# Kernel optimization log

Hardware: AMD Instinct MI355X
Metric: run time of the kernel (lower is better)

The kernel has to match this reference:

```python
import jax, jax.numpy as jnp
import numpy as np
from math import sqrt

B, L, D_MODEL = 4, 128, 256
V, D_WORD = 50257, 768
H = 8  # n_heads; d_keys = D_MODEL // H = 32


def setup_inputs() -> dict:
    key = jax.random.key(0)
    ks = jax.random.split(key, 10)
    s = lambda k, shape, fan: jax.random.normal(k, shape, dtype=jnp.float32) / np.sqrt(fan)
    return {
        "time_series_embedding": jax.random.normal(ks[0], (B, L, D_MODEL), dtype=jnp.float32),
        "word_embedding": jax.random.normal(ks[1], (V, D_WORD), dtype=jnp.float32) * 0.02,
        "Wq": s(ks[2], (D_MODEL, D_MODEL), D_MODEL),
        "bq": jnp.zeros((D_MODEL,), jnp.float32),
        "Wk": s(ks[3], (D_WORD, D_MODEL), D_WORD),
        "bk": jnp.zeros((D_MODEL,), jnp.float32),
        "Wv": s(ks[4], (D_WORD, D_MODEL), D_WORD),
        "bv": jnp.zeros((D_MODEL,), jnp.float32),
        "Wo": s(ks[5], (D_MODEL, D_MODEL), D_MODEL),
        "bo": jnp.zeros((D_MODEL,), jnp.float32),
    }


def reference(time_series_embedding, word_embedding, Wq, bq, Wk, bk, Wv, bv, Wo, bo):
    b, l, _ = time_series_embedding.shape
    v, _ = word_embedding.shape
    h = H
    e = D_MODEL // h
    # projections
    query = (time_series_embedding @ Wq + bq).reshape(b, l, h, e)   # [B,L,H,E]
    key = (word_embedding @ Wk + bk).reshape(v, h, e)               # [V,H,E]
    value = (word_embedding @ Wv + bv).reshape(v, h, e)             # [V,H,E]
    scale = 1.0 / sqrt(e)
    # scores over full vocab: [B,H,V,L]
    scores = jnp.einsum('blhe,vhe->bhvl', query, key)
    # NOTE: faithful to source -- softmax over the LAST axis (l, the query dim)
    attn = jax.nn.softmax(scale * scores, axis=-1)
    # dropout is identity in eval mode
    reprog = jnp.einsum('bhvl,vhe->blhe', attn, value).reshape(b, l, h * e)
    return reprog @ Wo + bo  # [B,L,d_model]
```

## Files before the change

kernel.cpp:

```cpp
#include <hip/hip_runtime.h>
#include <hip/hip_bf16.h>
#include <string.h>

#define BB 4
#define LL 128
#define DM 256
#define VV 50257
#define VPAD 50304
#define DW 768
#define HH 8
#define EE 32

typedef __attribute__((ext_vector_type(8))) short sh8;
typedef __attribute__((ext_vector_type(4))) short sh4;
typedef __attribute__((ext_vector_type(4))) float f32x4;

static __device__ inline unsigned short bfbits(float x) {
  __hip_bfloat16 h = __float2bfloat16(x);
  unsigned short u;
  __builtin_memcpy(&u, &h, 2);
  return u;
}

#define GLDS16(gsrc, ldst)                                                    \
  __builtin_amdgcn_global_load_lds(                                          \
      (const __attribute__((address_space(1))) void*)(gsrc),                 \
      (__attribute__((address_space(3))) void*)(ldst), 16, 0, 0)

#define WAIT_VM(N)                                                           \
  asm volatile("s_waitcnt vmcnt(" #N ")" ::: "memory");                      \
  __builtin_amdgcn_sched_barrier(0)
#define WAIT_LGKM0                                                           \
  asm volatile("s_waitcnt lgkmcnt(0)" ::: "memory");                         \
  __builtin_amdgcn_sched_barrier(0)

__global__ __launch_bounds__(256) void prep_kernel(
    const float* __restrict__ Wk, const float* __restrict__ Wv,
    unsigned short* __restrict__ Wkt, unsigned short* __restrict__ Wvt,
    const float* __restrict__ tse, const float* __restrict__ Wq,
    const float* __restrict__ bq, unsigned short* __restrict__ Qb) {
  __shared__ float tileS[64][65];
  int bid = blockIdx.x;
  int t = threadIdx.x;
  if (bid < 96) {
    int z = bid / 48, rem = bid - z * 48;
    int x = rem % 12, y = rem / 12;
    const float* src = z ? Wv : Wk;
    unsigned short* dst = z ? Wvt : Wkt;
    int k0 = x * 64, n0 = y * 64;
    int c = t & 63, rb = t >> 6;
#pragma unroll
    for (int j = 0; j < 16; ++j) {
      int r = j * 4 + rb;
      tileS[r][c] = src[(size_t)(k0 + r) * DM + n0 + c];
    }
    __syncthreads();
#pragma unroll
    for (int j = 0; j < 16; ++j) {
      int r = j * 4 + rb;
      dst[(size_t)(n0 + r) * DW + k0 + c] = bfbits(tileS[c][r]);
    }
  } else {
    int r = bid - 96;
    int n = t;
    float* row = &tileS[0][0];
    row[n] = tse[r * DM + n];
    __syncthreads();
    float acc = bq[n];
#pragma unroll 8
    for (int k = 0; k < DM; ++k)
      acc = fmaf(row[k], Wq[k * DM + n], acc);
    const float scale = 0.17677669529663687f * 1.4426950408889634f;
    Qb[r * DM + n] = bfbits(acc * scale);
  }
}

__global__ __launch_bounds__(256, 2) void kvproj_kernel(
    const float* __restrict__ WE, const unsigned short* __restrict__ Wkt,
    const unsigned short* __restrict__ Wvt, const float* __restrict__ bk,
    const float* __restrict__ bv, unsigned short* __restrict__ Kb,
    unsigned short* __restrict__ Vb) {
  __shared__ float WEf[2][128 * 32];
  __shared__ short Kbuf[2][128 * 32];
  __shared__ short Vbuf[2][128 * 32];

  int bx = blockIdx.x;
  int v0 = (bx >> 1) * 128;
  int colbase = (bx & 1) * 128;
  int t = threadIdx.x;
  int w = t >> 6, lane = t & 63, a = lane & 15, quad = lane >> 4;
  int wm = w >> 1, wn = w & 1;

  auto stage = [&](int kt, int p) {
#pragma unroll
    for (int i = 0; i < 4; ++i) {
      int s = w * 256 + i * 64 + lane;
      int row = s >> 3;
      int cc = (s & 7) ^ (row & 7);
      int grow = v0 + row;
      if (grow > VV - 1) grow = VV - 1;
      GLDS16(WE + (size_t)grow * DW + kt * 32 + cc * 4,
             &WEf[p][(w * 256 + i * 64) * 4]);
    }
#pragma unroll
    for (int i = 0; i < 2; ++i) {
      int s = w * 128 + i * 64 + lane;
      int row = s >> 2;
      int cc = (s & 3) ^ ((row >> 1) & 3);
      GLDS16(Wkt + (size_t)(colbase + row) * DW + kt * 32 + cc * 8,
             &Kbuf[p][(w * 128 + i * 64) * 8]);
      GLDS16(Wvt + (size_t)(colbase + row) * DW + kt * 32 + cc * 8,
             &Vbuf[p][(w * 128 + i * 64) * 8]);
    }
  };

  f32x4 Ck[4][4], Cv[4][4];
#pragma unroll
  for (int mb = 0; mb < 4; ++mb)
#pragma unroll
    for (int nb = 0; nb < 4; ++nb) {
      Ck[mb][nb] = (f32x4){0.f, 0.f, 0.f, 0.f};
      Cv[mb][nb] = (f32x4){0.f, 0.f, 0.f, 0.f};
    }

  stage(0, 0);
  stage(1, 1);

  for (int kt = 0; kt < 24; ++kt) {
    int p = kt & 1;
    if (kt < 23) {
      WAIT_VM(8);
    } else {
      WAIT_VM(0);
    }
    __builtin_amdgcn_s_barrier();
    __builtin_amdgcn_sched_barrier(0);

    sh8 A[4], Bk[4], Bv[4];
#pragma unroll
    for (int mb = 0; mb < 4; ++mb) {
      int row = wm * 64 + mb * 16 + a;
      const float* rp = &WEf[p][row * 32];
      f32x4 lo = *(const f32x4*)(rp + ((2 * quad) ^ (a & 7)) * 4);
      f32x4 hi = *(const f32x4*)(rp + ((2 * quad + 1) ^ (a & 7)) * 4);
      sh4 l4 = {(short)bfbits(lo[0]), (short)bfbits(lo[1]),
                (short)bfbits(lo[2]), (short)bfbits(lo[3])};
      sh4 h4 = {(short)bfbits(hi[0]), (short)bfbits(hi[1]),
                (short)bfbits(hi[2]), (short)bfbits(hi[3])};
      A[mb] = __builtin_shufflevector(l4, h4, 0, 1, 2, 3, 4, 5, 6, 7);
    }
#pragma unroll
    for (int nb = 0; nb < 4; ++nb) {
      int krow = (wn * 4 + nb) * 16 + a;
      int cp = (quad ^ ((krow >> 1) & 3)) * 8;
      Bk[nb] = *(const sh8*)&Kbuf[p][krow * 32 + cp];
      Bv[nb] = *(const sh8*)&Vbuf[p][krow * 32 + cp];
    }
#pragma unroll
    for (int mb = 0; mb < 4; ++mb)
#pragma unroll
      for (int nb = 0; nb < 4; ++nb) {
        Ck[mb][nb] = __builtin_amdgcn_mfma_f32_16x16x32_bf16(
            A[mb], Bk[nb], Ck[mb][nb], 0, 0, 0);
        Cv[mb][nb] = __builtin_amdgcn_mfma_f32_16x16x32_bf16(
            A[mb], Bv[nb], Cv[mb][nb], 0, 0, 0);
      }

    WAIT_LGKM0;
    __builtin_amdgcn_s_barrier();
    __builtin_amdgcn_sched_barrier(0);
    if (kt < 22) stage(kt + 2, p);
  }

  float bkv[4], bvv[4];
#pragma unroll
  for (int nb = 0; nb < 4; ++nb) {
    int n = colbase + (wn * 4 + nb) * 16 + a;
    bkv[nb] = bk[n];
    bvv[nb] = bv[n];
  }
#pragma unroll
  for (int mb = 0; mb < 4; ++mb)
#pragma unroll
    for (int nb = 0; nb < 4; ++nb)
#pragma unroll
      for (int r = 0; r < 4; ++r) {
        int m = v0 + wm * 64 + mb * 16 + quad * 4 + r;
        int n = colbase + (wn * 4 + nb) * 16 + a;
        bool ok = m < VV;
        Kb[(size_t)m * DM + n] = ok ? bfbits(Ck[mb][nb][r] + bkv[nb]) : 0;
        Vb[(size_t)m * DM + n] = ok ? bfbits(Cv[mb][nb][r] + bvv[nb]) : 0;
      }
}

#define PST 72
__global__ __launch_bounds__(256) void attn_kernel(
    const unsigned short* __restrict__ Qb, const unsigned short* __restrict__ Kb,
    const unsigned short* __restrict__ Vb, float* __restrict__ part, int bpb,
    int nc) {
  __shared__ short Pb[LL * PST];
  __shared__ short Vt[EE * PST];

  int bh = blockIdx.x / bpb;
  int chunk = blockIdx.x - bh * bpb;
  int b = bh >> 3, h = bh & 7;
  int t = threadIdx.x;
  int w = t >> 6;
  int lane = t & 63;
  int a = lane & 15;
  int quad = lane >> 4;
  int vr = t >> 2, e0 = (t & 3) * 8;

  sh8 qf[8];
  const unsigned short* qbase = Qb + (size_t)(b * LL) * DM + h * EE;
#pragma unroll
  for (int tau = 0; tau < 8; ++tau)
    qf[tau] = *(const sh8*)(qbase + (size_t)(tau * 16 + a) * DM + quad * 8);

  f32x4 C[2][2];
#pragma unroll
  for (int mb = 0; mb < 2; ++mb)
#pragma unroll
    for (int nb = 0; nb < 2; ++nb)
      C[mb][nb] = (f32x4){0.f, 0.f, 0.f, 0.f};

  const int ntiles = VPAD >> 6;

  sh8 af, vv;
  {
    int v0 = chunk << 6;
    af = *(const sh8*)(Kb + (size_t)(v0 + 16 * w + a) * DM + h * EE + quad * 8);
    vv = *(const sh8*)(Vb + (size_t)(v0 + vr) * DM + h * EE + e0);
  }

  for (int tile = chunk; tile < ntiles; tile += bpb) {
    f32x4 S[8];
#pragma unroll
    for (int tau = 0; tau < 8; ++tau) {
      f32x4 z = {0.f, 0.f, 0.f, 0.f};
      S[tau] = __builtin_amdgcn_mfma_f32_16x16x32_bf16(af, qf[tau], z, 0, 0, 0);
    }

    sh8 af2 = af, vv2 = vv;
    int nt = tile + bpb;
    if (nt < ntiles) {
      int v0n = nt << 6;
      af2 = *(const sh8*)(Kb + (size_t)(v0n + 16 * w + a) * DM + h * EE + quad * 8);
      vv2 = *(const sh8*)(Vb + (size_t)(v0n + vr) * DM + h * EE + e0);
    }

    float sm[4], inv[4];
#pragma unroll
    for (int r = 0; r < 4; ++r) sm[r] = 0.f;
#pragma unroll
    for (int tau = 0; tau < 8; ++tau)
#pragma unroll
      for (int r = 0; r < 4; ++r) {
        float ex = __builtin_amdgcn_exp2f(S[tau][r]);
        S[tau][r] = ex;
        sm[r] += ex;
      }
#pragma unroll
    for (int msk = 1; msk <= 8; msk <<= 1)
#pragma unroll
      for (int r = 0; r < 4; ++r)
        sm[r] += __shfl_xor(sm[r], msk);
#pragma unroll
    for (int r = 0; r < 4; ++r) inv[r] = 1.f / sm[r];

    WAIT_LGKM0;
    __builtin_amdgcn_s_barrier();
    __builtin_amdgcn_sched_barrier(0);

    {
      const short* vs = (const short*)&vv;
#pragma unroll
      for (int j = 0; j < 8; ++j)
        Vt[(e0 + j) * PST + vr] = vs[j];
    }
#pragma unroll
    for (int tau = 0; tau < 8; ++tau) {
      ushort4 pk;
      pk.x = bfbits(S[tau][0] * inv[0]);
      pk.y = bfbits(S[tau][1] * inv[1]);
      pk.z = bfbits(S[tau][2] * inv[2]);
      pk.w = bfbits(S[tau][3] * inv[3]);
      *(ushort4*)&Pb[(tau * 16 + a) * PST + 16 * w + quad * 4] = pk;
    }
    WAIT_LGKM0;
    __builtin_amdgcn_s_barrier();
    __builtin_amdgcn_sched_barrier(0);

    af = af2;
    vv = vv2;

    sh8 Afr[2][2], Bfr[2][2];
#pragma unroll
    for (int mb = 0; mb < 2; ++mb)
#pragma unroll
      for (int kb = 0; kb < 2; ++kb)
        Afr[mb][kb] =
            *(const sh8*)&Pb[(32 * w + mb * 16 + a) * PST + kb * 32 + quad * 8];
#pragma unroll
    for (int kb = 0; kb < 2; ++kb)
#pragma unroll
      for (int nb = 0; nb < 2; ++nb)
        Bfr[kb][nb] = *(const sh8*)&Vt[(nb * 16 + a) * PST + kb * 32 + quad * 8];
#pragma unroll
    for (int kb = 0; kb < 2; ++kb)
#pragma unroll
      for (int mb = 0; mb < 2; ++mb)
#pragma unroll
        for (int nb = 0; nb < 2; ++nb)
          C[mb][nb] = __builtin_amdgcn_mfma_f32_16x16x32_bf16(
              Afr[mb][kb], Bfr[kb][nb], C[mb][nb], 0, 0, 0);
  }

#pragma unroll
  for (int mb = 0; mb < 2; ++mb)
#pragma unroll
    for (int nb = 0; nb < 2; ++nb)
#pragma unroll
      for (int r = 0; r < 4; ++r) {
        int l = 32 * w + mb * 16 + quad * 4 + r;
        int e = nb * 16 + a;
        size_t idx = (size_t)(b * LL + l) * DM + h * EE + e;
        if (nc > 1)
          part[(size_t)chunk * (BB * LL * DM) + idx] = C[mb][nb][r];
        else
          atomicAdd(&part[idx], C[mb][nb][r]);
      }
}

__global__ __launch_bounds__(256) void outproj_kernel(
    const float* __restrict__ part, const float* __restrict__ Wo,
    const float* __restrict__ bo, float* __restrict__ out, int nc) {
  __shared__ float row[DM];
  int r = blockIdx.x, n = threadIdx.x;
  float s = 0.f;
  for (int c = 0; c < nc; ++c)
    s += part[(size_t)c * (BB * LL * DM) + (size_t)r * DM + n];
  row[n] = s;
  __syncthreads();
  float acc = bo[n];
#pragma unroll 8
  for (int k = 0; k < DM; ++k)
    acc = fmaf(row[k], Wo[k * DM + n], acc);
  out[r * DM + n] = acc;
}

extern "C" void kernel_launch(void* const* d_in, const int* in_sizes, int n_in,
                              void* d_out, int out_size, void* d_ws, size_t ws_size,
                              hipStream_t stream) {
  const float* tse = (const float*)d_in[0];
  const float* WE  = (const float*)d_in[1];
  const float* Wq  = (const float*)d_in[2];
  const float* bq  = (const float*)d_in[3];
  const float* Wk  = (const float*)d_in[4];
  const float* bk  = (const float*)d_in[5];
  const float* Wv  = (const float*)d_in[6];
  const float* bv  = (const float*)d_in[7];
  const float* Wo  = (const float*)d_in[8];
  const float* bo  = (const float*)d_in[9];
  float* out = (float*)d_out;

  char* ws = (char*)d_ws;
  const size_t QB_BYTES   = (size_t)BB * LL * DM * 2;
  const size_t KV_BYTES   = (size_t)VPAD * DM * 2;
  const size_t WT_BYTES   = (size_t)DM * DW * 2;
  const size_t PART_BYTES = (size_t)BB * LL * DM * 4;
  unsigned short* Qb  = (unsigned short*)ws;
  unsigned short* Kb  = (unsigned short*)(ws + QB_BYTES);
  unsigned short* Vb  = (unsigned short*)(ws + QB_BYTES + KV_BYTES);
  char* X = ws + QB_BYTES + 2 * KV_BYTES;
  unsigned short* Wkt = (unsigned short*)X;
  unsigned short* Wvt = (unsigned short*)(X + WT_BYTES);
  float* part = (float*)X;

  const int BPB = 32;

  const size_t NEED_PART =
      QB_BYTES + 2 * KV_BYTES + (size_t)BPB * PART_BYTES;
  const int nc = (ws_size >= NEED_PART) ? BPB : 1;

  prep_kernel<<<96 + BB * LL, 256, 0, stream>>>(Wk, Wv, Wkt, Wvt, tse, Wq, bq, Qb);
  kvproj_kernel<<<(VPAD / 128) * 2, 256, 0, stream>>>(WE, Wkt, Wvt, bk, bv, Kb, Vb);
  if (nc == 1)
    (void)hipMemsetAsync(part, 0, PART_BYTES, stream);
  attn_kernel<<<32 * BPB, 256, 0, stream>>>(Qb, Kb, Vb, part, BPB, nc);
  outproj_kernel<<<BB * LL, 256, 0, stream>>>(part, Wo, bo, out, nc);
}
```

Baseline: 401.4 us.

## Restructure K/V projection: direct global A loads, triple-buffered weights, smaller row tiles

The K/V projection kernel no longer stages word-embedding rows through LDS. Each lane loads its fp32 A-fragment straight from global memory and converts it to bf16 in registers. Weight tiles move to a three-slot LDS ring, which removes the second barrier per k-step, and the next stage is issued right after the barrier. The vocab tile drops from 128 to 64 rows, doubling the grid and allowing 3 blocks per CU, at the cost of reloading the weight tiles twice as often and doing uncoalesced-ish direct loads of the embedding.

Result: slower. 461.1 us (+14.9%).

```diff
diff --git a/kernel.cpp b/kernel.cpp
--- a/kernel.cpp
+++ b/kernel.cpp
@@ -28,10 +28,15 @@
       (__attribute__((address_space(3))) void*)(ldst), 16, 0, 0)
 
 #define WAIT_VM(N)                                                           \
+  __builtin_amdgcn_sched_barrier(0);                                         \
   asm volatile("s_waitcnt vmcnt(" #N ")" ::: "memory");                      \
   __builtin_amdgcn_sched_barrier(0)
 #define WAIT_LGKM0                                                           \
   asm volatile("s_waitcnt lgkmcnt(0)" ::: "memory");                         \
+  __builtin_amdgcn_sched_barrier(0)
+#define SBARRIER                                                             \
+  __builtin_amdgcn_sched_barrier(0);                                         \
+  __builtin_amdgcn_s_barrier();                                              \
   __builtin_amdgcn_sched_barrier(0)
 
 __global__ __launch_bounds__(256) void prep_kernel(
@@ -75,33 +80,22 @@
   }
 }
 
-__global__ __launch_bounds__(256, 2) void kvproj_kernel(
+__global__ __launch_bounds__(256, 3) void kvproj_kernel(
     const float* __restrict__ WE, const unsigned short* __restrict__ Wkt,
     const unsigned short* __restrict__ Wvt, const float* __restrict__ bk,
     const float* __restrict__ bv, unsigned short* __restrict__ Kb,
     unsigned short* __restrict__ Vb) {
-  __shared__ float WEf[2][128 * 32];
-  __shared__ short Kbuf[2][128 * 32];
-  __shared__ short Vbuf[2][128 * 32];
+  __shared__ short Kbuf[3][128 * 32];
+  __shared__ short Vbuf[3][128 * 32];
 
   int bx = blockIdx.x;
-  int v0 = (bx >> 1) * 128;
+  int v0 = (bx >> 1) * 64;
   int colbase = (bx & 1) * 128;
   int t = threadIdx.x;
   int w = t >> 6, lane = t & 63, a = lane & 15, quad = lane >> 4;
   int wm = w >> 1, wn = w & 1;
 
-  auto stage = [&](int kt, int p) {
-#pragma unroll
-    for (int i = 0; i < 4; ++i) {
-      int s = w * 256 + i * 64 + lane;
-      int row = s >> 3;
-      int cc = (s & 7) ^ (row & 7);
-      int grow = v0 + row;
-      if (grow > VV - 1) grow = VV - 1;
-      GLDS16(WE + (size_t)grow * DW + kt * 32 + cc * 4,
-             &WEf[p][(w * 256 + i * 64) * 4]);
-    }
+  auto stageKV = [&](int kt, int p) {
 #pragma unroll
     for (int i = 0; i < 2; ++i) {
       int s = w * 128 + i * 64 + lane;
@@ -114,50 +108,71 @@
     }
   };
 
-  f32x4 Ck[4][4], Cv[4][4];
-#pragma unroll
-  for (int mb = 0; mb < 4; ++mb)
+  const float* werow[2];
+#pragma unroll
+  for (int mb = 0; mb < 2; ++mb) {
+    int grow = v0 + wm * 32 + mb * 16 + a;
+    if (grow > VV - 1) grow = VV - 1;
+    werow[mb] = WE + (size_t)grow * DW + quad * 8;
+  }
+
+  f32x4 Ck[2][4], Cv[2][4];
+#pragma unroll
+  for (int mb = 0; mb < 2; ++mb)
 #pragma unroll
     for (int nb = 0; nb < 4; ++nb) {
       Ck[mb][nb] = (f32x4){0.f, 0.f, 0.f, 0.f};
       Cv[mb][nb] = (f32x4){0.f, 0.f, 0.f, 0.f};
     }
 
-  stage(0, 0);
-  stage(1, 1);
-
+  stageKV(0, 0);
+  stageKV(1, 1);
+
+  int p = 0;
   for (int kt = 0; kt < 24; ++kt) {
-    int p = kt & 1;
     if (kt < 23) {
-      WAIT_VM(8);
+      WAIT_VM(4);
     } else {
       WAIT_VM(0);
     }
-    __builtin_amdgcn_s_barrier();
+    SBARRIER;
+
+    f32x4 lo0 = *(const f32x4*)(werow[0] + kt * 32);
+    f32x4 hi0 = *(const f32x4*)(werow[0] + kt * 32 + 4);
+    f32x4 lo1 = *(const f32x4*)(werow[1] + kt * 32);
+    f32x4 hi1 = *(const f32x4*)(werow[1] + kt * 32 + 4);
     __builtin_amdgcn_sched_barrier(0);
 
-    sh8 A[4], Bk[4], Bv[4];
-#pragma unroll
-    for (int mb = 0; mb < 4; ++mb) {
-      int row = wm * 64 + mb * 16 + a;
-      const float* rp = &WEf[p][row * 32];
-      f32x4 lo = *(const f32x4*)(rp + ((2 * quad) ^ (a & 7)) * 4);
-      f32x4 hi = *(const f32x4*)(rp + ((2 * quad + 1) ^ (a & 7)) * 4);
-      sh4 l4 = {(short)bfbits(lo[0]), (short)bfbits(lo[1]),
-                (short)bfbits(lo[2]), (short)bfbits(lo[3])};
-      sh4 h4 = {(short)bfbits(hi[0]), (short)bfbits(hi[1]),
-                (short)bfbits(hi[2]), (short)bfbits(hi[3])};
-      A[mb] = __builtin_shufflevector(l4, h4, 0, 1, 2, 3, 4, 5, 6, 7);
-    }
+    {
+      int q = p - 1;
+      if (q < 0) q = 2;
+      if (kt < 22) stageKV(kt + 2, q);
+    }
+
+    sh8 A[2];
+    {
+      sh4 l4 = {(short)bfbits(lo0[0]), (short)bfbits(lo0[1]),
+                (short)bfbits(lo0[2]), (short)bfbits(lo0[3])};
+      sh4 h4 = {(short)bfbits(hi0[0]), (short)bfbits(hi0[1]),
+                (short)bfbits(hi0[2]), (short)bfbits(hi0[3])};
+      A[0] = __builtin_shufflevector(l4, h4, 0, 1, 2, 3, 4, 5, 6, 7);
+      sh4 l5 = {(short)bfbits(lo1[0]), (short)bfbits(lo1[1]),
+                (short)bfbits(lo1[2]), (short)bfbits(lo1[3])};
+      sh4 h5 = {(short)bfbits(hi1[0]), (short)bfbits(hi1[1]),
+                (short)bfbits(hi1[2]), (short)bfbits(hi1[3])};
+      A[1] = __builtin_shufflevector(l5, h5, 0, 1, 2, 3, 4, 5, 6, 7);
+    }
+
+    sh8 Bk[4], Bv[4];
 #pragma unroll
     for (int nb = 0; nb < 4; ++nb) {
-      int krow = (wn * 4 + nb) * 16 + a;
+      int krow = wn * 64 + nb * 16 + a;
       int cp = (quad ^ ((krow >> 1) & 3)) * 8;
       Bk[nb] = *(const sh8*)&Kbuf[p][krow * 32 + cp];
       Bv[nb] = *(const sh8*)&Vbuf[p][krow * 32 + cp];
     }
 #pragma unroll
-    for (int mb = 0; mb < 4; ++mb)
+    for (int mb = 0; mb < 2; ++mb)
 #pragma unroll
       for (int nb = 0; nb < 4; ++nb) {
         Ck[mb][nb] = __builtin_amdgcn_mfma_f32_16x16x32_bf16(
@@ -166,27 +181,24 @@
             A[mb], Bv[nb], Cv[mb][nb], 0, 0, 0);
       }
 
-    WAIT_LGKM0;
-    __builtin_amdgcn_s_barrier();
-    __builtin_amdgcn_sched_barrier(0);
-    if (kt < 22) stage(kt + 2, p);
+    p = (p == 2) ? 0 : p + 1;
   }
 
   float bkv[4], bvv[4];
 #pragma unroll
   for (int nb = 0; nb < 4; ++nb) {
-    int n = colbase + (wn * 4 + nb) * 16 + a;
+    int n = colbase + wn * 64 + nb * 16 + a;
     bkv[nb] = bk[n];
     bvv[nb] = bv[n];
   }
 #pragma unroll
-  for (int mb = 0; mb < 4; ++mb)
+  for (int mb = 0; mb < 2; ++mb)
 #pragma unroll
     for (int nb = 0; nb < 4; ++nb)
 #pragma unroll
       for (int r = 0; r < 4; ++r) {
-        int m = v0 + wm * 64 + mb * 16 + quad * 4 + r;
-        int n = colbase + (wn * 4 + nb) * 16 + a;
+        int m = v0 + wm * 32 + mb * 16 + quad * 4 + r;
+        int n = colbase + wn * 64 + nb * 16 + a;
         bool ok = m < VV;
         Kb[(size_t)m * DM + n] = ok ? bfbits(Ck[mb][nb][r] + bkv[nb]) : 0;
         Vb[(size_t)m * DM + n] = ok ? bfbits(Cv[mb][nb][r] + bvv[nb]) : 0;
@@ -269,8 +281,7 @@
     for (int r = 0; r < 4; ++r) inv[r] = 1.f / sm[r];
 
     WAIT_LGKM0;
-    __builtin_amdgcn_s_barrier();
-    __builtin_amdgcn_sched_barrier(0);
+    SBARRIER;
 
     {
       const short* vs = (const short*)&vv;
@@ -288,8 +299,7 @@
       *(ushort4*)&Pb[(tau * 16 + a) * PST + 16 * w + quad * 4] = pk;
     }
     WAIT_LGKM0;
-    __builtin_amdgcn_s_barrier();
-    __builtin_amdgcn_sched_barrier(0);
+    SBARRIER;
 
     af = af2;
     vv = vv2;
@@ -384,7 +394,7 @@
   const int nc = (ws_size >= NEED_PART) ? BPB : 1;
 
   prep_kernel<<<96 + BB * LL, 256, 0, stream>>>(Wk, Wv, Wkt, Wvt, tse, Wq, bq, Qb);
-  kvproj_kernel<<<(VPAD / 128) * 2, 256, 0, stream>>>(WE, Wkt, Wvt, bk, bv, Kb, Vb);
+  kvproj_kernel<<<(VPAD / 64) * 2, 256, 0, stream>>>(WE, Wkt, Wvt, bk, bv, Kb, Vb);
   if (nc == 1)
     (void)hipMemsetAsync(part, 0, PART_BYTES, stream);
   attn_kernel<<<32 * BPB, 256, 0, stream>>>(Qb, Kb, Vb, part, BPB, nc);
```

## Store V transposed and keep P in registers for attention PV MFMA

Applied to the files above, without the earlier changes.

The K/V projection kernel now writes V transposed (feature-major over the padded vocab), so the attention kernel can load V fragments straight from global memory. The softmax probabilities stay in registers and feed 16x16x16 bf16 MFMAs directly. This removes the shared-memory staging of P and V and the two block barriers per tile. In exchange, each wave accumulates partial outputs for all 128 queries, which must be reduced across the four waves through shared memory at the end. The kvproj epilogue now does strided 8-byte stores of V^T.

Result: no change. 408.7 us (+1.8%).

```diff
diff --git a/kernel.cpp b/kernel.cpp
--- a/kernel.cpp
+++ b/kernel.cpp
@@ -28,11 +28,29 @@
       (__attribute__((address_space(3))) void*)(ldst), 16, 0, 0)
 
 #define WAIT_VM(N)                                                           \
+  __builtin_amdgcn_sched_barrier(0);                                         \
   asm volatile("s_waitcnt vmcnt(" #N ")" ::: "memory");                      \
   __builtin_amdgcn_sched_barrier(0)
 #define WAIT_LGKM0                                                           \
   asm volatile("s_waitcnt lgkmcnt(0)" ::: "memory");                         \
   __builtin_amdgcn_sched_barrier(0)
+#define SBARRIER                                                             \
+  __builtin_amdgcn_sched_barrier(0);                                         \
+  __builtin_amdgcn_s_barrier();                                              \
+  __builtin_amdgcn_sched_barrier(0)
+
+#if __has_builtin(__builtin_amdgcn_mfma_f32_16x16x16bf16_1k)
+#define MFMA16(A, B, C) __builtin_amdgcn_mfma_f32_16x16x16bf16_1k(A, B, C, 0, 0, 0)
+#elif __has_builtin(__builtin_amdgcn_mfma_f32_16x16x16_bf16)
+#define MFMA16(A, B, C) __builtin_amdgcn_mfma_f32_16x16x16_bf16(A, B, C, 0, 0, 0)
+#else
+static __device__ inline f32x4 mfma16_asm(sh4 a, sh4 b, f32x4 c) {
+  asm volatile("v_mfma_f32_16x16x16_bf16 %0, %1, %2, %0"
+               : "+v"(c) : "v"(a), "v"(b));
+  return c;
+}
+#define MFMA16(A, B, C) mfma16_asm(A, B, C)
+#endif
 
 __global__ __launch_bounds__(256) void prep_kernel(
     const float* __restrict__ Wk, const float* __restrict__ Wv,
@@ -79,7 +97,7 @@
     const float* __restrict__ WE, const unsigned short* __restrict__ Wkt,
     const unsigned short* __restrict__ Wvt, const float* __restrict__ bk,
     const float* __restrict__ bv, unsigned short* __restrict__ Kb,
-    unsigned short* __restrict__ Vb) {
+    unsigned short* __restrict__ Vbt) {
   __shared__ float WEf[2][128 * 32];
   __shared__ short Kbuf[2][128 * 32];
   __shared__ short Vbuf[2][128 * 32];
@@ -133,8 +151,7 @@
     } else {
       WAIT_VM(0);
     }
-    __builtin_amdgcn_s_barrier();
-    __builtin_amdgcn_sched_barrier(0);
+    SBARRIER;
 
     sh8 A[4], Bk[4], Bv[4];
 #pragma unroll
@@ -167,8 +184,7 @@
       }
 
     WAIT_LGKM0;
-    __builtin_amdgcn_s_barrier();
-    __builtin_amdgcn_sched_barrier(0);
+    SBARRIER;
     if (kt < 22) stage(kt + 2, p);
   }
 
@@ -182,24 +198,26 @@
 #pragma unroll
   for (int mb = 0; mb < 4; ++mb)
 #pragma unroll
-    for (int nb = 0; nb < 4; ++nb)
+    for (int nb = 0; nb < 4; ++nb) {
+      int m0 = v0 + wm * 64 + mb * 16 + quad * 4;
+      int n = colbase + (wn * 4 + nb) * 16 + a;
+      sh4 vq;
 #pragma unroll
       for (int r = 0; r < 4; ++r) {
-        int m = v0 + wm * 64 + mb * 16 + quad * 4 + r;
-        int n = colbase + (wn * 4 + nb) * 16 + a;
+        int m = m0 + r;
         bool ok = m < VV;
         Kb[(size_t)m * DM + n] = ok ? bfbits(Ck[mb][nb][r] + bkv[nb]) : 0;
-        Vb[(size_t)m * DM + n] = ok ? bfbits(Cv[mb][nb][r] + bvv[nb]) : 0;
+        vq[r] = ok ? (short)bfbits(Cv[mb][nb][r] + bvv[nb]) : (short)0;
       }
-}
-
-#define PST 72
+      *(sh4*)&Vbt[(size_t)n * VPAD + m0] = vq;
+    }
+}
+
 __global__ __launch_bounds__(256) void attn_kernel(
     const unsigned short* __restrict__ Qb, const unsigned short* __restrict__ Kb,
-    const unsigned short* __restrict__ Vb, float* __restrict__ part, int bpb,
+    const unsigned short* __restrict__ Vbt, float* __restrict__ part, int bpb,
     int nc) {
-  __shared__ short Pb[LL * PST];
-  __shared__ short Vt[EE * PST];
+  __shared__ float Cred[4][32][129];
 
   int bh = blockIdx.x / bpb;
   int chunk = blockIdx.x - bh * bpb;
@@ -209,7 +227,6 @@
   int lane = t & 63;
   int a = lane & 15;
   int quad = lane >> 4;
-  int vr = t >> 2, e0 = (t & 3) * 8;
 
   sh8 qf[8];
   const unsigned short* qbase = Qb + (size_t)(b * LL) * DM + h * EE;
@@ -217,20 +234,24 @@
   for (int tau = 0; tau < 8; ++tau)
     qf[tau] = *(const sh8*)(qbase + (size_t)(tau * 16 + a) * DM + quad * 8);
 
-  f32x4 C[2][2];
-#pragma unroll
-  for (int mb = 0; mb < 2; ++mb)
-#pragma unroll
-    for (int nb = 0; nb < 2; ++nb)
-      C[mb][nb] = (f32x4){0.f, 0.f, 0.f, 0.f};
+  f32x4 C2[2][8];
+#pragma unroll
+  for (int nb = 0; nb < 2; ++nb)
+#pragma unroll
+    for (int tau = 0; tau < 8; ++tau)
+      C2[nb][tau] = (f32x4){0.f, 0.f, 0.f, 0.f};
 
   const int ntiles = VPAD >> 6;
 
-  sh8 af, vv;
+  sh8 af;
+  sh4 av[2];
   {
     int v0 = chunk << 6;
     af = *(const sh8*)(Kb + (size_t)(v0 + 16 * w + a) * DM + h * EE + quad * 8);
-    vv = *(const sh8*)(Vb + (size_t)(v0 + vr) * DM + h * EE + e0);
+#pragma unroll
+    for (int nb = 0; nb < 2; ++nb)
+      av[nb] = *(const sh4*)(Vbt + (size_t)(h * EE + nb * 16 + a) * VPAD +
+                             v0 + 16 * w + quad * 4);
   }
 
   for (int tile = chunk; tile < ntiles; tile += bpb) {
@@ -241,12 +262,16 @@
       S[tau] = __builtin_amdgcn_mfma_f32_16x16x32_bf16(af, qf[tau], z, 0, 0, 0);
     }
 
-    sh8 af2 = af, vv2 = vv;
+    sh8 af2 = af;
+    sh4 av2[2] = {av[0], av[1]};
     int nt = tile + bpb;
     if (nt < ntiles) {
       int v0n = nt << 6;
       af2 = *(const sh8*)(Kb + (size_t)(v0n + 16 * w + a) * DM + h * EE + quad * 8);
-      vv2 = *(const sh8*)(Vb + (size_t)(v0n + vr) * DM + h * EE + e0);
+#pragma unroll
+      for (int nb = 0; nb < 2; ++nb)
+        av2[nb] = *(const sh4*)(Vbt + (size_t)(h * EE + nb * 16 + a) * VPAD +
+                                v0n + 16 * w + quad * 4);
     }
 
     float sm[4], inv[4];
@@ -268,68 +293,45 @@
 #pragma unroll
     for (int r = 0; r < 4; ++r) inv[r] = 1.f / sm[r];
 
-    WAIT_LGKM0;
-    __builtin_amdgcn_s_barrier();
-    __builtin_amdgcn_sched_barrier(0);
-
-    {
-      const short* vs = (const short*)&vv;
-#pragma unroll
-      for (int j = 0; j < 8; ++j)
-        Vt[(e0 + j) * PST + vr] = vs[j];
-    }
+    sh4 pb[8];
 #pragma unroll
     for (int tau = 0; tau < 8; ++tau) {
-      ushort4 pk;
-      pk.x = bfbits(S[tau][0] * inv[0]);
-      pk.y = bfbits(S[tau][1] * inv[1]);
-      pk.z = bfbits(S[tau][2] * inv[2]);
-      pk.w = bfbits(S[tau][3] * inv[3]);
-      *(ushort4*)&Pb[(tau * 16 + a) * PST + 16 * w + quad * 4] = pk;
-    }
-    WAIT_LGKM0;
-    __builtin_amdgcn_s_barrier();
-    __builtin_amdgcn_sched_barrier(0);
+      pb[tau][0] = (short)bfbits(S[tau][0] * inv[0]);
+      pb[tau][1] = (short)bfbits(S[tau][1] * inv[1]);
+      pb[tau][2] = (short)bfbits(S[tau][2] * inv[2]);
+      pb[tau][3] = (short)bfbits(S[tau][3] * inv[3]);
+    }
+
+#pragma unroll
+    for (int nb = 0; nb < 2; ++nb)
+#pragma unroll
+      for (int tau = 0; tau < 8; ++tau)
+        C2[nb][tau] = MFMA16(av[nb], pb[tau], C2[nb][tau]);
 
     af = af2;
-    vv = vv2;
-
-    sh8 Afr[2][2], Bfr[2][2];
-#pragma unroll
-    for (int mb = 0; mb < 2; ++mb)
-#pragma unroll
-      for (int kb = 0; kb < 2; ++kb)
-        Afr[mb][kb] =
-            *(const sh8*)&Pb[(32 * w + mb * 16 + a) * PST + kb * 32 + quad * 8];
-#pragma unroll
-    for (int kb = 0; kb < 2; ++kb)
-#pragma unroll
-      for (int nb = 0; nb < 2; ++nb)
-        Bfr[kb][nb] = *(const sh8*)&Vt[(nb * 16 + a) * PST + kb * 32 + quad * 8];
-#pragma unroll
-    for (int kb = 0; kb < 2; ++kb)
-#pragma unroll
-      for (int mb = 0; mb < 2; ++mb)
-#pragma unroll
-        for (int nb = 0; nb < 2; ++nb)
-          C[mb][nb] = __builtin_amdgcn_mfma_f32_16x16x32_bf16(
-              Afr[mb][kb], Bfr[kb][nb], C[mb][nb], 0, 0, 0);
-  }
-
-#pragma unroll
-  for (int mb = 0; mb < 2; ++mb)
-#pragma unroll
-    for (int nb = 0; nb < 2; ++nb)
-#pragma unroll
-      for (int r = 0; r < 4; ++r) {
-        int l = 32 * w + mb * 16 + quad * 4 + r;
-        int e = nb * 16 + a;
-        size_t idx = (size_t)(b * LL + l) * DM + h * EE + e;
-        if (nc > 1)
-          part[(size_t)chunk * (BB * LL * DM) + idx] = C[mb][nb][r];
-        else
-          atomicAdd(&part[idx], C[mb][nb][r]);
-      }
+    av[0] = av2[0];
+    av[1] = av2[1];
+  }
+
+#pragma unroll
+  for (int nb = 0; nb < 2; ++nb)
+#pragma unroll
+    for (int tau = 0; tau < 8; ++tau)
+#pragma unroll
+      for (int r = 0; r < 4; ++r)
+        Cred[w][nb * 16 + quad * 4 + r][tau * 16 + a] = C2[nb][tau][r];
+  __syncthreads();
+#pragma unroll
+  for (int j = 0; j < 16; ++j) {
+    int f = t + 256 * j;
+    int e = f & 31, l = f >> 5;
+    float s = Cred[0][e][l] + Cred[1][e][l] + Cred[2][e][l] + Cred[3][e][l];
+    size_t idx = (size_t)(b * LL + l) * DM + h * EE + e;
+    if (nc > 1)
+      part[(size_t)chunk * (BB * LL * DM) + idx] = s;
+    else
+      atomicAdd(&part[idx], s);
+  }
 }
 
 __global__ __launch_bounds__(256) void outproj_kernel(
@@ -371,7 +373,7 @@
   const size_t PART_BYTES = (size_t)BB * LL * DM * 4;
   unsigned short* Qb  = (unsigned short*)ws;
   unsigned short* Kb  = (unsigned short*)(ws + QB_BYTES);
-  unsigned short* Vb  = (unsigned short*)(ws + QB_BYTES + KV_BYTES);
+  unsigned short* Vbt = (unsigned short*)(ws + QB_BYTES + KV_BYTES);
   char* X = ws + QB_BYTES + 2 * KV_BYTES;
   unsigned short* Wkt = (unsigned short*)X;
   unsigned short* Wvt = (unsigned short*)(X + WT_BYTES);
@@ -384,9 +386,9 @@
   const int nc = (ws_size >= NEED_PART) ? BPB : 1;
 
   prep_kernel<<<96 + BB * LL, 256, 0, stream>>>(Wk, Wv, Wkt, Wvt, tse, Wq, bq, Qb);
-  kvproj_kernel<<<(VPAD / 128) * 2, 256, 0, stream>>>(WE, Wkt, Wvt, bk, bv, Kb, Vb);
+  kvproj_kernel<<<(VPAD / 128) * 2, 256, 0, stream>>>(WE, Wkt, Wvt, bk, bv, Kb, Vbt);
   if (nc == 1)
     (void)hipMemsetAsync(part, 0, PART_BYTES, stream);
-  attn_kernel<<<32 * BPB, 256, 0, stream>>>(Qb, Kb, Vb, part, BPB, nc);
+  attn_kernel<<<32 * BPB, 256, 0, stream>>>(Qb, Kb, Vbt, part, BPB, nc);
   outproj_kernel<<<BB * LL, 256, 0, stream>>>(part, Wo, bo, out, nc);
 }
```
